# Kernel optimization log

Hardware: AMD Instinct MI355X
Metric: run time of the kernel (lower is better)

Reference implementation:

```python
import jax, jax.numpy as jnp
import numpy as np

B, N, D, H = 256, 32768, 1024, 16
DH = D // H

def setup_inputs() -> dict:
    key = jax.random.key(0)
    ks = jax.random.split(key, 6)
    scale = 1.0 / np.sqrt(D)  # xavier-ish scale for weights
    return {
        "q": jax.random.normal(ks[0], (B, D), jnp.float32),
        "k": jax.random.normal(ks[1], (N, D), jnp.float32),
        "v": jax.random.normal(ks[2], (N, D), jnp.float32),
        "W_q": jax.random.normal(ks[3], (D, D), jnp.float32) * scale,
        "W_k": jax.random.normal(ks[4], (D, D), jnp.float32) * scale,
        "W_v": jax.random.normal(ks[5], (D, D), jnp.float32) * scale,
    }

def reference(q, k, v, W_q, W_k, W_v):
    # nn.Linear(x) = x @ W.T (no bias)
    qh = (q @ W_q.T).reshape(B, H, DH)   # [B,H,dh]
    kh = (k @ W_k.T).reshape(N, H, DH)   # [N,H,dh]
    vh = (v @ W_v.T).reshape(N, H, DH)   # [N,H,dh]
    inv_sqrt_dh = 1.0 / np.sqrt(DH).astype(np.float32)
    # decode-style cross attention: single query per (head, batch) over N keys
    score = jnp.einsum('bhd,nhd->hbn', qh, kh) * inv_sqrt_dh  # [H,B,N]
    weights = jax.nn.softmax(score, axis=-1)                   # [H,B,N]
    # dropout is identity in eval mode
    context = jnp.einsum('hbn,nhd->bhd', weights, vh)          # [B,H,dh]
    return context.reshape(B, D)
```

## Files before the change

### kernel.cpp

```cpp
#include <hip/hip_runtime.h>
#include <hip/hip_bf16.h>

#define B_  256
#define N_  32768
#define D_  1024
#define H_  16
#define DH_ 64
#define NSPLIT 8

typedef __attribute__((ext_vector_type(8))) short bf16x8;
typedef __attribute__((ext_vector_type(4))) float f32x4;

static __device__ __forceinline__ short f2bf(float f) {
    union { __hip_bfloat16 h; short s; } u;
    u.h = __float2bfloat16(f);
    return u.s;
}

__global__ __launch_bounds__(256, 2)
void proj_gemm(const float* __restrict__ A, const float* __restrict__ W,
               short* __restrict__ C, int M, int K, int Dout, float alpha)
{
    __shared__ short As[128 * 40];
    __shared__ short Ws[128 * 40];

    const int tid  = threadIdx.x;
    const int wave = tid >> 6;
    const int lane = tid & 63;
    const int quad = lane >> 4;
    const int l16  = lane & 15;

    const int block_n = blockIdx.x * 128;
    const int block_m = blockIdx.y * 128;
    const int wm = (wave & 1) * 64;
    const int wn = (wave >> 1) * 64;

    f32x4 acc[4][4];
#pragma unroll
    for (int i = 0; i < 4; ++i)
#pragma unroll
        for (int j = 0; j < 4; ++j) acc[i][j] = (f32x4){0.f, 0.f, 0.f, 0.f};

    for (int kt = 0; kt < K; kt += 32) {
        __syncthreads();
#pragma unroll
        for (int it = 0; it < 4; ++it) {
            int s  = it * 256 + tid;
            int r  = s >> 3;
            int c4 = s & 7;
            float4 va = *(const float4*)(A + (size_t)(block_m + r) * K + kt + c4 * 4);
            float4 vw = *(const float4*)(W + (size_t)(block_n + r) * K + kt + c4 * 4);
            short4 ha = make_short4(f2bf(va.x), f2bf(va.y), f2bf(va.z), f2bf(va.w));
            short4 hw = make_short4(f2bf(vw.x), f2bf(vw.y), f2bf(vw.z), f2bf(vw.w));
            *(short4*)&As[r * 40 + c4 * 4] = ha;
            *(short4*)&Ws[r * 40 + c4 * 4] = hw;
        }
        __syncthreads();

        bf16x8 afrag[4], bfrag[4];
#pragma unroll
        for (int mi = 0; mi < 4; ++mi)
            afrag[mi] = *(const bf16x8*)&As[(wm + mi * 16 + l16) * 40 + quad * 8];
#pragma unroll
        for (int ni = 0; ni < 4; ++ni)
            bfrag[ni] = *(const bf16x8*)&Ws[(wn + ni * 16 + l16) * 40 + quad * 8];
#pragma unroll
        for (int mi = 0; mi < 4; ++mi)
#pragma unroll
            for (int ni = 0; ni < 4; ++ni)
                acc[mi][ni] = __builtin_amdgcn_mfma_f32_16x16x32_bf16(
                    afrag[mi], bfrag[ni], acc[mi][ni], 0, 0, 0);
    }

#pragma unroll
    for (int mi = 0; mi < 4; ++mi)
#pragma unroll
        for (int ni = 0; ni < 4; ++ni)
#pragma unroll
            for (int reg = 0; reg < 4; ++reg) {
                int r = block_m + wm + mi * 16 + quad * 4 + reg;
                int c = block_n + wn + ni * 16 + l16;
                C[(size_t)r * Dout + c] = f2bf(acc[mi][ni][reg] * alpha);
            }
}

__global__ __launch_bounds__(256, 2)
void attn_kernel(const short* __restrict__ qh, const short* __restrict__ kh,
                 const short* __restrict__ vhT, float* __restrict__ partO,
                 float* __restrict__ partM, float* __restrict__ partL)
{
    const int ns = blockIdx.x, qt = blockIdx.y, h = blockIdx.z;
    const int tid  = threadIdx.x;
    const int wave = tid >> 6;
    const int lane = tid & 63;
    const int quad = lane >> 4;
    const int l16  = lane & 15;

    __shared__ short Ks[64][72];
    __shared__ short Vt[64][72];
    __shared__ short Ps[4][16][72];

    const int qrow = qt * 64 + wave * 16 + l16;
    bf16x8 aQ[2];
    aQ[0] = *(const bf16x8*)(qh + (size_t)qrow * D_ + h * DH_ + quad * 8);
    aQ[1] = *(const bf16x8*)(qh + (size_t)qrow * D_ + h * DH_ + 32 + quad * 8);

    f32x4 ofrag[4];
#pragma unroll
    for (int dt = 0; dt < 4; ++dt) ofrag[dt] = (f32x4){0.f, 0.f, 0.f, 0.f};
    float m_i[4], l_i[4];
#pragma unroll
    for (int r = 0; r < 4; ++r) { m_i[r] = -__builtin_inff(); l_i[r] = 0.f; }

    const int nPer = N_ / NSPLIT;
    const int n0 = ns * nPer;

    for (int ch = 0; ch < nPer; ch += 64) {
        const int nb = n0 + ch;
        __syncthreads();
#pragma unroll
        for (int it = 0; it < 2; ++it) {
            int s  = it * 256 + tid;
            int r  = s >> 3;
            int c8 = s & 7;
            *(bf16x8*)&Ks[r][c8 * 8] =
                *(const bf16x8*)(kh + (size_t)(nb + r) * D_ + h * DH_ + c8 * 8);
            *(bf16x8*)&Vt[r][c8 * 8] =
                *(const bf16x8*)(vhT + (size_t)(h * DH_ + r) * N_ + nb + c8 * 8);
        }
        __syncthreads();

        f32x4 sfrag[4];
#pragma unroll
        for (int nt = 0; nt < 4; ++nt) sfrag[nt] = (f32x4){0.f, 0.f, 0.f, 0.f};
#pragma unroll
        for (int ks = 0; ks < 2; ++ks)
#pragma unroll
            for (int nt = 0; nt < 4; ++nt) {
                bf16x8 bK = *(const bf16x8*)&Ks[nt * 16 + l16][ks * 32 + quad * 8];
                sfrag[nt] = __builtin_amdgcn_mfma_f32_16x16x32_bf16(
                    aQ[ks], bK, sfrag[nt], 0, 0, 0);
            }

        float cmax[4];
#pragma unroll
        for (int r = 0; r < 4; ++r)
            cmax[r] = fmaxf(fmaxf(sfrag[0][r], sfrag[1][r]),
                            fmaxf(sfrag[2][r], sfrag[3][r]));
#pragma unroll
        for (int off = 1; off < 16; off <<= 1)
#pragma unroll
            for (int r = 0; r < 4; ++r)
                cmax[r] = fmaxf(cmax[r], __shfl_xor(cmax[r], off));

        float alpha[4], psum[4];
#pragma unroll
        for (int r = 0; r < 4; ++r) {
            float mn = fmaxf(m_i[r], cmax[r]);
            alpha[r] = __expf(m_i[r] - mn);
            m_i[r] = mn;
            psum[r] = 0.f;
        }
#pragma unroll
        for (int nt = 0; nt < 4; ++nt)
#pragma unroll
            for (int r = 0; r < 4; ++r) {
                float p = __expf(sfrag[nt][r] - m_i[r]);
                psum[r] += p;
                Ps[wave][quad * 4 + r][nt * 16 + l16] = f2bf(p);
            }
#pragma unroll
        for (int off = 1; off < 16; off <<= 1)
#pragma unroll
            for (int r = 0; r < 4; ++r) psum[r] += __shfl_xor(psum[r], off);
#pragma unroll
        for (int r = 0; r < 4; ++r) l_i[r] = l_i[r] * alpha[r] + psum[r];
#pragma unroll
        for (int dt = 0; dt < 4; ++dt)
#pragma unroll
            for (int r = 0; r < 4; ++r) ofrag[dt][r] *= alpha[r];

#pragma unroll
        for (int ks = 0; ks < 2; ++ks) {
            bf16x8 aP = *(const bf16x8*)&Ps[wave][l16][ks * 32 + quad * 8];
#pragma unroll
            for (int dt = 0; dt < 4; ++dt) {
                bf16x8 bV = *(const bf16x8*)&Vt[dt * 16 + l16][ks * 32 + quad * 8];
                ofrag[dt] = __builtin_amdgcn_mfma_f32_16x16x32_bf16(
                    aP, bV, ofrag[dt], 0, 0, 0);
            }
        }
    }

    const int bid = (h * 4 + qt) * NSPLIT + ns;
    float* Ob = partO + (size_t)bid * 4096;
#pragma unroll
    for (int dt = 0; dt < 4; ++dt)
#pragma unroll
        for (int r = 0; r < 4; ++r)
            Ob[(wave * 16 + quad * 4 + r) * 64 + dt * 16 + l16] = ofrag[dt][r];
    if (l16 == 0) {
#pragma unroll
        for (int r = 0; r < 4; ++r) {
            partM[bid * 64 + wave * 16 + quad * 4 + r] = m_i[r];
            partL[bid * 64 + wave * 16 + quad * 4 + r] = l_i[r];
        }
    }
}

__global__ __launch_bounds__(256)
void merge_kernel(const float* __restrict__ partO, const float* __restrict__ partM,
                  const float* __restrict__ partL, float* __restrict__ out)
{
    int idx = blockIdx.x * 256 + threadIdx.x;
    int b   = idx >> 10;
    int col = idx & 1023;
    int h   = col >> 6;
    int d   = col & 63;
    int qt  = b >> 6;
    int rin = b & 63;
    int base = (h * 4 + qt) * NSPLIT;

    float mmax = -__builtin_inff();
#pragma unroll
    for (int s = 0; s < NSPLIT; ++s)
        mmax = fmaxf(mmax, partM[(base + s) * 64 + rin]);
    float L = 0.f, o = 0.f;
#pragma unroll
    for (int s = 0; s < NSPLIT; ++s) {
        float c = __expf(partM[(base + s) * 64 + rin] - mmax);
        L += c * partL[(base + s) * 64 + rin];
        o += c * partO[(size_t)(base + s) * 4096 + rin * 64 + d];
    }
    out[idx] = o / L;
}

extern "C" void kernel_launch(void* const* d_in, const int* in_sizes, int n_in,
                              void* d_out, int out_size, void* d_ws, size_t ws_size,
                              hipStream_t stream) {
    const float* q   = (const float*)d_in[0];
    const float* k   = (const float*)d_in[1];
    const float* v   = (const float*)d_in[2];
    const float* W_q = (const float*)d_in[3];
    const float* W_k = (const float*)d_in[4];
    const float* W_v = (const float*)d_in[5];
    float* out = (float*)d_out;

    short* qh  = (short*)d_ws;
    short* kh  = qh + (size_t)B_ * D_;
    short* vhT = kh + (size_t)N_ * D_;
    float* partO = (float*)(vhT + (size_t)D_ * N_);
    float* partM = partO + (size_t)512 * 4096;
    float* partL = partM + (size_t)512 * 64;

    dim3 blk(256);
    const float inv_sqrt_dh = 0.125f;

    proj_gemm<<<dim3(8, 2), blk, 0, stream>>>(q, W_q, qh, B_, D_, D_, inv_sqrt_dh);
    proj_gemm<<<dim3(8, 256), blk, 0, stream>>>(k, W_k, kh, N_, D_, D_, 1.0f);
    proj_gemm<<<dim3(256, 8), blk, 0, stream>>>(W_v, v, vhT, D_, D_, N_, 1.0f);

    attn_kernel<<<dim3(NSPLIT, 4, 16), blk, 0, stream>>>(qh, kh, vhT,
                                                         partO, partM, partL);
    merge_kernel<<<dim3((B_ * D_) / 256), blk, 0, stream>>>(partO, partM, partL, out);
}
```

Measured before the change: 709.8 us.

## Pre-convert weights to bf16, XCD-aware GEMM tiling, register-resident K/V attention

Adds a pre-pass that converts the weight matrices to bf16 so the projection GEMMs load bf16 weight tiles directly instead of converting fp32 twice per tile. It also remaps GEMM block IDs so that blocks on the same XCD share input rows. The attention kernel now drops LDS staging for K and V, loads fragments straight into registers with K prefetched one chunk ahead, and gives each wave 32 queries with a 16-way key split. The merge is adapted to the new partial layout. The costs are extra launches, more workspace and higher register pressure, and the unpadded LDS stride of 32 may cause bank conflicts.

```diff
diff --git a/kernel.cpp b/kernel.cpp
--- a/kernel.cpp
+++ b/kernel.cpp
@@ -6,7 +6,8 @@
 #define D_  1024
 #define H_  16
 #define DH_ 64
-#define NSPLIT 8
+#define KSPLIT 16
+#define STRIPE (N_ / KSPLIT)
 
 typedef __attribute__((ext_vector_type(8))) short bf16x8;
 typedef __attribute__((ext_vector_type(4))) float f32x4;
@@ -17,12 +18,23 @@
     return u.s;
 }
 
+__global__ __launch_bounds__(256)
+void f2b_kernel(const float* __restrict__ in, short* __restrict__ out, int n4)
+{
+    int i = blockIdx.x * 256 + threadIdx.x;
+    if (i < n4) {
+        float4 v = ((const float4*)in)[i];
+        ((short4*)out)[i] = make_short4(f2bf(v.x), f2bf(v.y), f2bf(v.z), f2bf(v.w));
+    }
+}
+
+template<bool SWAP>
 __global__ __launch_bounds__(256, 2)
-void proj_gemm(const float* __restrict__ A, const float* __restrict__ W,
-               short* __restrict__ C, int M, int K, int Dout, float alpha)
+void gemm_hybrid(const float* __restrict__ P, const short* __restrict__ Qb,
+                 short* __restrict__ C, int MP, int MQ, int K, int ldc, float alpha)
 {
-    __shared__ short As[128 * 40];
-    __shared__ short Ws[128 * 40];
+    __shared__ __align__(16) short Pf[128 * 32];
+    __shared__ __align__(16) short Qs[128 * 32];
 
     const int tid  = threadIdx.x;
     const int wave = tid >> 6;
@@ -30,8 +42,15 @@
     const int quad = lane >> 4;
     const int l16  = lane & 15;
 
-    const int block_n = blockIdx.x * 128;
-    const int block_m = blockIdx.y * 128;
+    const int gp = MP >> 7, gq = MQ >> 7;
+    const int bid = blockIdx.x;
+    int bp, bq;
+    if (gp >= 8) {
+        int xcd = bid & 7, w = bid >> 3, sp = gp >> 3;
+        bp = xcd * sp + w / gq;
+        bq = w % gq;
+    } else { bp = bid / gq; bq = bid % gq; }
+
     const int wm = (wave & 1) * 64;
     const int wn = (wave >> 1) * 64;
 
@@ -45,42 +64,47 @@
         __syncthreads();
 #pragma unroll
         for (int it = 0; it < 4; ++it) {
-            int s  = it * 256 + tid;
-            int r  = s >> 3;
-            int c4 = s & 7;
-            float4 va = *(const float4*)(A + (size_t)(block_m + r) * K + kt + c4 * 4);
-            float4 vw = *(const float4*)(W + (size_t)(block_n + r) * K + kt + c4 * 4);
-            short4 ha = make_short4(f2bf(va.x), f2bf(va.y), f2bf(va.z), f2bf(va.w));
-            short4 hw = make_short4(f2bf(vw.x), f2bf(vw.y), f2bf(vw.z), f2bf(vw.w));
-            *(short4*)&As[r * 40 + c4 * 4] = ha;
-            *(short4*)&Ws[r * 40 + c4 * 4] = hw;
+            int s = it * 256 + tid, r = s >> 3, c4 = s & 7;
+            float4 v = *(const float4*)(P + (size_t)(bp * 128 + r) * K + kt + c4 * 4);
+            *(short4*)&Pf[r * 32 + c4 * 4] =
+                make_short4(f2bf(v.x), f2bf(v.y), f2bf(v.z), f2bf(v.w));
+        }
+#pragma unroll
+        for (int it = 0; it < 2; ++it) {
+            int s = it * 256 + tid, r = s >> 2, c8 = s & 3;
+            *(bf16x8*)&Qs[r * 32 + c8 * 8] =
+                *(const bf16x8*)(Qb + (size_t)(bq * 128 + r) * K + kt + c8 * 8);
         }
         __syncthreads();
 
-        bf16x8 afrag[4], bfrag[4];
+        const short* LA = SWAP ? Qs : Pf;
+        const short* LB = SWAP ? Pf : Qs;
+        bf16x8 af[4], bf[4];
 #pragma unroll
         for (int mi = 0; mi < 4; ++mi)
-            afrag[mi] = *(const bf16x8*)&As[(wm + mi * 16 + l16) * 40 + quad * 8];
+            af[mi] = *(const bf16x8*)&LA[(wm + mi * 16 + l16) * 32 + quad * 8];
 #pragma unroll
         for (int ni = 0; ni < 4; ++ni)
-            bfrag[ni] = *(const bf16x8*)&Ws[(wn + ni * 16 + l16) * 40 + quad * 8];
+            bf[ni] = *(const bf16x8*)&LB[(wn + ni * 16 + l16) * 32 + quad * 8];
 #pragma unroll
         for (int mi = 0; mi < 4; ++mi)
 #pragma unroll
             for (int ni = 0; ni < 4; ++ni)
                 acc[mi][ni] = __builtin_amdgcn_mfma_f32_16x16x32_bf16(
-                    afrag[mi], bfrag[ni], acc[mi][ni], 0, 0, 0);
-    }
-
+                    af[mi], bf[ni], acc[mi][ni], 0, 0, 0);
+    }
+
+    const int rb = (SWAP ? bq : bp) * 128;
+    const int cb = (SWAP ? bp : bq) * 128;
 #pragma unroll
     for (int mi = 0; mi < 4; ++mi)
 #pragma unroll
         for (int ni = 0; ni < 4; ++ni)
 #pragma unroll
             for (int reg = 0; reg < 4; ++reg) {
-                int r = block_m + wm + mi * 16 + quad * 4 + reg;
-                int c = block_n + wn + ni * 16 + l16;
-                C[(size_t)r * Dout + c] = f2bf(acc[mi][ni][reg] * alpha);
+                int r = rb + wm + mi * 16 + quad * 4 + reg;
+                int c = cb + wn + ni * 16 + l16;
+                C[(size_t)r * ldc + c] = f2bf(acc[mi][ni][reg] * alpha);
             }
 }
 
@@ -89,121 +113,131 @@
                  const short* __restrict__ vhT, float* __restrict__ partO,
                  float* __restrict__ partM, float* __restrict__ partL)
 {
-    const int ns = blockIdx.x, qt = blockIdx.y, h = blockIdx.z;
+    const int st = blockIdx.x, qb2 = blockIdx.y, h = blockIdx.z;
     const int tid  = threadIdx.x;
     const int wave = tid >> 6;
     const int lane = tid & 63;
     const int quad = lane >> 4;
     const int l16  = lane & 15;
 
-    __shared__ short Ks[64][72];
-    __shared__ short Vt[64][72];
-    __shared__ short Ps[4][16][72];
-
-    const int qrow = qt * 64 + wave * 16 + l16;
-    bf16x8 aQ[2];
-    aQ[0] = *(const bf16x8*)(qh + (size_t)qrow * D_ + h * DH_ + quad * 8);
-    aQ[1] = *(const bf16x8*)(qh + (size_t)qrow * D_ + h * DH_ + 32 + quad * 8);
-
-    f32x4 ofrag[4];
-#pragma unroll
-    for (int dt = 0; dt < 4; ++dt) ofrag[dt] = (f32x4){0.f, 0.f, 0.f, 0.f};
-    float m_i[4], l_i[4];
-#pragma unroll
-    for (int r = 0; r < 4; ++r) { m_i[r] = -__builtin_inff(); l_i[r] = 0.f; }
-
-    const int nPer = N_ / NSPLIT;
-    const int n0 = ns * nPer;
-
-    for (int ch = 0; ch < nPer; ch += 64) {
+    __shared__ __align__(16) short Ps[4][32][72];
+
+    const int qbase = qb2 * 128 + wave * 32;
+    const int hoff  = h * DH_;
+
+    bf16x8 qfr[2][2];
+#pragma unroll
+    for (int qf = 0; qf < 2; ++qf)
+#pragma unroll
+        for (int ks = 0; ks < 2; ++ks)
+            qfr[qf][ks] = *(const bf16x8*)(qh + (size_t)(qbase + qf * 16 + l16) * D_
+                                           + hoff + ks * 32 + quad * 8);
+
+    f32x4 ofrag[2][4];
+#pragma unroll
+    for (int qf = 0; qf < 2; ++qf)
+#pragma unroll
+        for (int dt = 0; dt < 4; ++dt) ofrag[qf][dt] = (f32x4){0.f, 0.f, 0.f, 0.f};
+    float m_i[2] = {-__builtin_inff(), -__builtin_inff()};
+    float l_i[2] = {0.f, 0.f};
+
+    const int n0 = st * STRIPE;
+
+    bf16x8 akf[4][2];
+#pragma unroll
+    for (int kf = 0; kf < 4; ++kf)
+#pragma unroll
+        for (int ks = 0; ks < 2; ++ks)
+            akf[kf][ks] = *(const bf16x8*)(kh + (size_t)(n0 + kf * 16 + l16) * D_
+                                           + hoff + ks * 32 + quad * 8);
+
+    for (int ch = 0; ch < STRIPE; ch += 64) {
         const int nb = n0 + ch;
-        __syncthreads();
-#pragma unroll
-        for (int it = 0; it < 2; ++it) {
-            int s  = it * 256 + tid;
-            int r  = s >> 3;
-            int c8 = s & 7;
-            *(bf16x8*)&Ks[r][c8 * 8] =
-                *(const bf16x8*)(kh + (size_t)(nb + r) * D_ + h * DH_ + c8 * 8);
-            *(bf16x8*)&Vt[r][c8 * 8] =
-                *(const bf16x8*)(vhT + (size_t)(h * DH_ + r) * N_ + nb + c8 * 8);
+
+        f32x4 sf[4][2];
+#pragma unroll
+        for (int kf = 0; kf < 4; ++kf)
+#pragma unroll
+            for (int qf = 0; qf < 2; ++qf) sf[kf][qf] = (f32x4){0.f, 0.f, 0.f, 0.f};
+#pragma unroll
+        for (int ks = 0; ks < 2; ++ks)
+#pragma unroll
+            for (int kf = 0; kf < 4; ++kf)
+#pragma unroll
+                for (int qf = 0; qf < 2; ++qf)
+                    sf[kf][qf] = __builtin_amdgcn_mfma_f32_16x16x32_bf16(
+                        akf[kf][ks], qfr[qf][ks], sf[kf][qf], 0, 0, 0);
+
+        bf16x8 avf[4][2];
+#pragma unroll
+        for (int dt = 0; dt < 4; ++dt)
+#pragma unroll
+            for (int g = 0; g < 2; ++g)
+                avf[dt][g] = *(const bf16x8*)(vhT + (size_t)(hoff + dt * 16 + l16) * N_
+                                              + nb + g * 32 + quad * 8);
+
+        const int nbn = (ch + 64 < STRIPE) ? nb + 64 : nb;
+#pragma unroll
+        for (int kf = 0; kf < 4; ++kf)
+#pragma unroll
+            for (int ks = 0; ks < 2; ++ks)
+                akf[kf][ks] = *(const bf16x8*)(kh + (size_t)(nbn + kf * 16 + l16) * D_
+                                               + hoff + ks * 32 + quad * 8);
+
+#pragma unroll
+        for (int qf = 0; qf < 2; ++qf) {
+            float mx = sf[0][qf][0];
+#pragma unroll
+            for (int kf = 0; kf < 4; ++kf)
+#pragma unroll
+                for (int r = 0; r < 4; ++r) mx = fmaxf(mx, sf[kf][qf][r]);
+            mx = fmaxf(mx, __shfl_xor(mx, 16));
+            mx = fmaxf(mx, __shfl_xor(mx, 32));
+            float mn = fmaxf(m_i[qf], mx);
+            float al = __expf(m_i[qf] - mn);
+            m_i[qf] = mn;
+            float ps = 0.f;
+#pragma unroll
+            for (int kf = 0; kf < 4; ++kf) {
+                float p0 = __expf(sf[kf][qf][0] - mn);
+                float p1 = __expf(sf[kf][qf][1] - mn);
+                float p2 = __expf(sf[kf][qf][2] - mn);
+                float p3 = __expf(sf[kf][qf][3] - mn);
+                ps += (p0 + p1) + (p2 + p3);
+                *(short4*)&Ps[wave][qf * 16 + l16][kf * 16 + quad * 4] =
+                    make_short4(f2bf(p0), f2bf(p1), f2bf(p2), f2bf(p3));
+            }
+            ps += __shfl_xor(ps, 16);
+            ps += __shfl_xor(ps, 32);
+            l_i[qf] = l_i[qf] * al + ps;
+#pragma unroll
+            for (int dt = 0; dt < 4; ++dt) ofrag[qf][dt] *= al;
         }
-        __syncthreads();
-
-        f32x4 sfrag[4];
-#pragma unroll
-        for (int nt = 0; nt < 4; ++nt) sfrag[nt] = (f32x4){0.f, 0.f, 0.f, 0.f};
-#pragma unroll
-        for (int ks = 0; ks < 2; ++ks)
-#pragma unroll
-            for (int nt = 0; nt < 4; ++nt) {
-                bf16x8 bK = *(const bf16x8*)&Ks[nt * 16 + l16][ks * 32 + quad * 8];
-                sfrag[nt] = __builtin_amdgcn_mfma_f32_16x16x32_bf16(
-                    aQ[ks], bK, sfrag[nt], 0, 0, 0);
+
+#pragma unroll
+        for (int qf = 0; qf < 2; ++qf)
+#pragma unroll
+            for (int g = 0; g < 2; ++g) {
+                bf16x8 bP = *(const bf16x8*)&Ps[wave][qf * 16 + l16][g * 32 + quad * 8];
+#pragma unroll
+                for (int dt = 0; dt < 4; ++dt)
+                    ofrag[qf][dt] = __builtin_amdgcn_mfma_f32_16x16x32_bf16(
+                        avf[dt][g], bP, ofrag[qf][dt], 0, 0, 0);
             }
-
-        float cmax[4];
-#pragma unroll
-        for (int r = 0; r < 4; ++r)
-            cmax[r] = fmaxf(fmaxf(sfrag[0][r], sfrag[1][r]),
-                            fmaxf(sfrag[2][r], sfrag[3][r]));
-#pragma unroll
-        for (int off = 1; off < 16; off <<= 1)
-#pragma unroll
-            for (int r = 0; r < 4; ++r)
-                cmax[r] = fmaxf(cmax[r], __shfl_xor(cmax[r], off));
-
-        float alpha[4], psum[4];
-#pragma unroll
-        for (int r = 0; r < 4; ++r) {
-            float mn = fmaxf(m_i[r], cmax[r]);
-            alpha[r] = __expf(m_i[r] - mn);
-            m_i[r] = mn;
-            psum[r] = 0.f;
-        }
-#pragma unroll
-        for (int nt = 0; nt < 4; ++nt)
-#pragma unroll
-            for (int r = 0; r < 4; ++r) {
-                float p = __expf(sfrag[nt][r] - m_i[r]);
-                psum[r] += p;
-                Ps[wave][quad * 4 + r][nt * 16 + l16] = f2bf(p);
-            }
-#pragma unroll
-        for (int off = 1; off < 16; off <<= 1)
-#pragma unroll
-            for (int r = 0; r < 4; ++r) psum[r] += __shfl_xor(psum[r], off);
-#pragma unroll
-        for (int r = 0; r < 4; ++r) l_i[r] = l_i[r] * alpha[r] + psum[r];
+    }
+
+    const int pid = ((h * KSPLIT + st) * 2 + qb2) * 4 + wave;
+#pragma unroll
+    for (int qf = 0; qf < 2; ++qf)
 #pragma unroll
         for (int dt = 0; dt < 4; ++dt)
-#pragma unroll
-            for (int r = 0; r < 4; ++r) ofrag[dt][r] *= alpha[r];
-
-#pragma unroll
-        for (int ks = 0; ks < 2; ++ks) {
-            bf16x8 aP = *(const bf16x8*)&Ps[wave][l16][ks * 32 + quad * 8];
-#pragma unroll
-            for (int dt = 0; dt < 4; ++dt) {
-                bf16x8 bV = *(const bf16x8*)&Vt[dt * 16 + l16][ks * 32 + quad * 8];
-                ofrag[dt] = __builtin_amdgcn_mfma_f32_16x16x32_bf16(
-                    aP, bV, ofrag[dt], 0, 0, 0);
-            }
-        }
-    }
-
-    const int bid = (h * 4 + qt) * NSPLIT + ns;
-    float* Ob = partO + (size_t)bid * 4096;
-#pragma unroll
-    for (int dt = 0; dt < 4; ++dt)
-#pragma unroll
-        for (int r = 0; r < 4; ++r)
-            Ob[(wave * 16 + quad * 4 + r) * 64 + dt * 16 + l16] = ofrag[dt][r];
-    if (l16 == 0) {
-#pragma unroll
-        for (int r = 0; r < 4; ++r) {
-            partM[bid * 64 + wave * 16 + quad * 4 + r] = m_i[r];
-            partL[bid * 64 + wave * 16 + quad * 4 + r] = l_i[r];
+            *(f32x4*)&partO[((size_t)pid * 32 + qf * 16 + l16) * 64 + dt * 16 + quad * 4]
+                = ofrag[qf][dt];
+    if (quad == 0) {
+#pragma unroll
+        for (int qf = 0; qf < 2; ++qf) {
+            partM[pid * 32 + qf * 16 + l16] = m_i[qf];
+            partL[pid * 32 + qf * 16 + l16] = l_i[qf];
         }
     }
 }
@@ -217,20 +251,22 @@
     int col = idx & 1023;
     int h   = col >> 6;
     int d   = col & 63;
-    int qt  = b >> 6;
-    int rin = b & 63;
-    int base = (h * 4 + qt) * NSPLIT;
+    int blk32 = b >> 5, rin = b & 31;
+    int qb2 = blk32 >> 2, w = blk32 & 3;
 
     float mmax = -__builtin_inff();
 #pragma unroll
-    for (int s = 0; s < NSPLIT; ++s)
-        mmax = fmaxf(mmax, partM[(base + s) * 64 + rin]);
+    for (int st = 0; st < KSPLIT; ++st) {
+        int pid = ((h * KSPLIT + st) * 2 + qb2) * 4 + w;
+        mmax = fmaxf(mmax, partM[pid * 32 + rin]);
+    }
     float L = 0.f, o = 0.f;
 #pragma unroll
-    for (int s = 0; s < NSPLIT; ++s) {
-        float c = __expf(partM[(base + s) * 64 + rin] - mmax);
-        L += c * partL[(base + s) * 64 + rin];
-        o += c * partO[(size_t)(base + s) * 4096 + rin * 64 + d];
+    for (int st = 0; st < KSPLIT; ++st) {
+        int pid = ((h * KSPLIT + st) * 2 + qb2) * 4 + w;
+        float c = __expf(partM[pid * 32 + rin] - mmax);
+        L += c * partL[pid * 32 + rin];
+        o += c * partO[((size_t)pid * 32 + rin) * 64 + d];
     }
     out[idx] = o / L;
 }
@@ -247,20 +283,26 @@
     float* out = (float*)d_out;
 
     short* qh  = (short*)d_ws;
-    short* kh  = qh + (size_t)B_ * D_;
-    short* vhT = kh + (size_t)N_ * D_;
-    float* partO = (float*)(vhT + (size_t)D_ * N_);
-    float* partM = partO + (size_t)512 * 4096;
-    float* partL = partM + (size_t)512 * 64;
+    short* kh  = qh  + (size_t)B_ * D_;
+    short* vhT = kh  + (size_t)N_ * D_;
+    short* Wqb = vhT + (size_t)D_ * N_;
+    short* Wkb = Wqb + (size_t)D_ * D_;
+    short* Wvb = Wkb + (size_t)D_ * D_;
+    float* partO = (float*)(Wvb + (size_t)D_ * D_);
+    float* partM = partO + (size_t)2048 * 32 * 64;
+    float* partL = partM + (size_t)2048 * 32;
 
     dim3 blk(256);
-    const float inv_sqrt_dh = 0.125f;
-
-    proj_gemm<<<dim3(8, 2), blk, 0, stream>>>(q, W_q, qh, B_, D_, D_, inv_sqrt_dh);
-    proj_gemm<<<dim3(8, 256), blk, 0, stream>>>(k, W_k, kh, N_, D_, D_, 1.0f);
-    proj_gemm<<<dim3(256, 8), blk, 0, stream>>>(W_v, v, vhT, D_, D_, N_, 1.0f);
-
-    attn_kernel<<<dim3(NSPLIT, 4, 16), blk, 0, stream>>>(qh, kh, vhT,
-                                                         partO, partM, partL);
+    const int w4 = (D_ * D_) / 4;
+
+    f2b_kernel<<<dim3(w4 / 256), blk, 0, stream>>>(W_q, Wqb, w4);
+    f2b_kernel<<<dim3(w4 / 256), blk, 0, stream>>>(W_k, Wkb, w4);
+    f2b_kernel<<<dim3(w4 / 256), blk, 0, stream>>>(W_v, Wvb, w4);
+
+    gemm_hybrid<false><<<dim3(2 * 8), blk, 0, stream>>>(q, Wqb, qh, B_, D_, D_, D_, 0.125f);
+    gemm_hybrid<false><<<dim3(256 * 8), blk, 0, stream>>>(k, Wkb, kh, N_, D_, D_, D_, 1.0f);
+    gemm_hybrid<true><<<dim3(256 * 8), blk, 0, stream>>>(v, Wvb, vhT, N_, D_, D_, N_, 1.0f);
+
+    attn_kernel<<<dim3(KSPLIT, 2, H_), blk, 0, stream>>>(qh, kh, vhT, partO, partM, partL);
     merge_kernel<<<dim3((B_ * D_) / 256), blk, 0, stream>>>(partO, partM, partL, out);
 }
```

Measured after the change: 651.0 us. 1.09x faster.
